# Kernel tuning notes

Measured on AMD Instinct MI355X. Metric: run time of the kernel, lower is better.

The kernel has to match this reference:

```python
import jax, jax.numpy as jnp
import numpy as np

N_NODES = 100000
N_EDGES = 1600000
D = 128


def setup_inputs() -> dict:
    key = jax.random.key(0)
    k1, k2, k3, k4 = jax.random.split(key, 4)
    x = jax.random.normal(k1, (N_NODES, D), dtype=jnp.float32)
    edge_index = jax.random.randint(k2, (2, N_EDGES), 0, N_NODES, dtype=jnp.int32)
    # torch.nn.Linear(nfeat, nclass): weight [out, in], bias [out]
    W = jax.random.normal(k3, (D, D), dtype=jnp.float32) * (1.0 / np.sqrt(D))
    b = jax.random.normal(k4, (D,), dtype=jnp.float32) * 0.01
    return {"x": x, "edge_index": edge_index, "W": W, "b": b}


def reference(x, edge_index, W, b):
    n = x.shape[0]
    # gcn_norm: add self-loops, edge_weight = 1
    loop = jnp.arange(n, dtype=edge_index.dtype)
    row = jnp.concatenate([edge_index[0], loop])  # source
    col = jnp.concatenate([edge_index[1], loop])  # target
    deg = jax.ops.segment_sum(jnp.ones_like(col, dtype=x.dtype), col, num_segments=n)
    dinv = jnp.where(deg > 0, deg ** -0.5, 0.0)
    norm = dinv[row] * dinv[col]  # [E+N]
    # K=1 propagate: out[col] += norm * x[row]
    agg = jax.ops.segment_sum(x[row] * norm[:, None], col, num_segments=n)
    # linear (y = agg @ W^T + b), then relu + residual
    h = agg @ W.T + b
    return x + jax.nn.relu(h)
```

## Files before the change

kernel.cpp:

```cpp
#include <hip/hip_runtime.h>

#define NN 100000
#define NE 1600000
#define DD 128
#define NBLK 98
#define NBUK 782
#define NB_AC 256
#define CHUNK 6250
#define SCAN_N (NBUK * NB_AC)
#define NB_SCAN 196
#define NB_YG ((NN + 63) / 64)

typedef __attribute__((ext_vector_type(8))) short bf16x8;
typedef __attribute__((ext_vector_type(4))) float f32x4;
typedef __attribute__((ext_vector_type(2))) float f32x2;

__device__ __forceinline__ float bf2f(unsigned short u) {
    return __uint_as_float(((unsigned)u) << 16);
}
__device__ __forceinline__ unsigned short f2bf(float f) {
    unsigned u = __float_as_uint(f);
    u += 0x7FFFu + ((u >> 16) & 1u);
    return (unsigned short)(u >> 16);
}

__global__ __launch_bounds__(1024) void k_hist(const int* __restrict__ col,
                                               unsigned* __restrict__ part) {
    __shared__ unsigned hist[NBUK];
    int t = threadIdx.x, blk = blockIdx.x;
    for (int i = t; i < NBUK; i += 1024) hist[i] = 0;
    __syncthreads();
    int beg = blk * CHUNK, end = beg + CHUNK;
    for (int e = beg + t; e < end; e += 1024)
        atomicAdd(&hist[col[e] >> 7], 1u);
    __syncthreads();
    for (int i = t; i < NBUK; i += 1024)
        part[(size_t)i * NB_AC + blk] = hist[i];
}

__global__ __launch_bounds__(1024) void k_bsum(const unsigned* __restrict__ part,
                                               unsigned* __restrict__ sb) {
    __shared__ unsigned red[1024];
    int t = threadIdx.x;
    int i = blockIdx.x * 1024 + t;
    red[t] = i < SCAN_N ? part[i] : 0;
    __syncthreads();
    for (int off = 512; off > 0; off >>= 1) {
        if (t < off) red[t] += red[t + off];
        __syncthreads();
    }
    if (t == 0) sb[blockIdx.x] = red[0];
}

__global__ __launch_bounds__(1024) void k_scanpart(const unsigned* __restrict__ part,
                                                   const unsigned* __restrict__ sb,
                                                   unsigned* __restrict__ off) {
    __shared__ unsigned s2[256];
    __shared__ unsigned s[1024];
    int t = threadIdx.x;
    if (t < 256) s2[t] = (t < NB_SCAN) ? sb[t] : 0;
    __syncthreads();
    for (int o = 1; o < 256; o <<= 1) {
        unsigned v = 0;
        if (t < 256 && t >= o) v = s2[t - o];
        __syncthreads();
        if (t < 256) s2[t] += v;
        __syncthreads();
    }
    unsigned boff = blockIdx.x == 0 ? 0 : s2[blockIdx.x - 1];
    int i = blockIdx.x * 1024 + t;
    unsigned v = i < SCAN_N ? part[i] : 0;
    s[t] = v;
    __syncthreads();
    for (int o = 1; o < 1024; o <<= 1) {
        unsigned u = t >= o ? s[t - o] : 0;
        __syncthreads();
        s[t] += u;
        __syncthreads();
    }
    if (i < SCAN_N) off[i] = boff + s[t] - v;
}

__global__ __launch_bounds__(1024) void k_scatter_pk(const int* __restrict__ row,
                                                     const int* __restrict__ col,
                                                     const unsigned* __restrict__ off,
                                                     unsigned* __restrict__ packed) {
    __shared__ unsigned cur[NBUK];
    int t = threadIdx.x, blk = blockIdx.x;
    for (int i = t; i < NBUK; i += 1024) cur[i] = off[(size_t)i * NB_AC + blk];
    __syncthreads();
    int beg = blk * CHUNK, end = beg + CHUNK;
    for (int e = beg + t; e < end; e += 1024) {
        int c = col[e];
        unsigned pos = atomicAdd(&cur[c >> 7], 1u);
        packed[pos] = ((unsigned)(c & 127) << 17) | (unsigned)row[e];
    }
}

__global__ __launch_bounds__(256) void k_finalize(const unsigned* __restrict__ off,
                                                  const unsigned* __restrict__ packed,
                                                  float* __restrict__ dinv,
                                                  int* __restrict__ rowptr,
                                                  int* __restrict__ esrc,
                                                  const float* __restrict__ x,
                                                  const float* __restrict__ W,
                                                  unsigned char* __restrict__ yb8) {
    __shared__ unsigned short wb[DD * DD];
    __shared__ unsigned deg[128], pre[128], tmp[128];
    int t = threadIdx.x;

    if (blockIdx.x < NBUK) {
        int buk = blockIdx.x;
        unsigned bstart = off[(size_t)buk * NB_AC];
        unsigned bend = (buk == NBUK - 1) ? (unsigned)NE : off[(size_t)(buk + 1) * NB_AC];
        if (t < 128) deg[t] = 0;
        __syncthreads();
        for (unsigned e = bstart + t; e < bend; e += 256)
            atomicAdd(&deg[packed[e] >> 17], 1u);
        __syncthreads();
        if (t < 128) tmp[t] = deg[t];
        __syncthreads();
        for (int o = 1; o < 128; o <<= 1) {
            unsigned v = 0;
            if (t < 128 && t >= o) v = tmp[t - o];
            __syncthreads();
            if (t < 128) tmp[t] += v;
            __syncthreads();
        }
        if (t < 128) {
            pre[t] = tmp[t] - deg[t];
            int n = buk * 128 + t;
            if (n < NN) {
                dinv[n] = 1.0f / sqrtf((float)(deg[t] + 1));
                rowptr[n] = (int)(bstart + pre[t]);
            }
        }
        if (buk == NBUK - 1 && t == 0) rowptr[NN] = NE;
        __syncthreads();
        if (t < 128) deg[t] = pre[t];
        __syncthreads();
        for (unsigned e = bstart + t; e < bend; e += 256) {
            unsigned p = packed[e];
            unsigned pos = atomicAdd(&deg[p >> 17], 1u);
            esrc[bstart + pos] = (int)(p & 0x1FFFFu);
        }
    } else {
        int blk = blockIdx.x - NBUK;
#pragma unroll
        for (int it = 0; it < 8; ++it) {
            int unit = t + 256 * it;
            int wrow = unit >> 4;
            int c0 = (unit & 15) * 8;
            float4 v0 = *(const float4*)(W + wrow * DD + c0);
            float4 v1 = *(const float4*)(W + wrow * DD + c0 + 4);
            bf16x8 h;
            h[0] = (short)f2bf(v0.x); h[1] = (short)f2bf(v0.y);
            h[2] = (short)f2bf(v0.z); h[3] = (short)f2bf(v0.w);
            h[4] = (short)f2bf(v1.x); h[5] = (short)f2bf(v1.y);
            h[6] = (short)f2bf(v1.z); h[7] = (short)f2bf(v1.w);
            int byte = (wrow * 256 + c0 * 2) ^ ((wrow & 7) << 4);
            *(bf16x8*)((char*)wb + byte) = h;
        }
        __syncthreads();

        int wave = t >> 6;
        int lane = t & 63;
        int lrow = lane & 15;
        int kg = lane >> 4;

        int arow = blk * 64 + wave * 16 + lrow;
        int arc = arow < NN ? arow : NN - 1;
        bf16x8 afrag[4];
#pragma unroll
        for (int ks = 0; ks < 4; ++ks) {
            const float* src = x + (size_t)arc * DD + ks * 32 + kg * 8;
            float4 v0 = *(const float4*)src;
            float4 v1 = *(const float4*)(src + 4);
            bf16x8 h;
            h[0] = (short)f2bf(v0.x); h[1] = (short)f2bf(v0.y);
            h[2] = (short)f2bf(v0.z); h[3] = (short)f2bf(v0.w);
            h[4] = (short)f2bf(v1.x); h[5] = (short)f2bf(v1.y);
            h[6] = (short)f2bf(v1.z); h[7] = (short)f2bf(v1.w);
            afrag[ks] = h;
        }

        f32x4 acc[8];
#pragma unroll
        for (int ct = 0; ct < 8; ++ct) acc[ct] = (f32x4)(0.f);

#pragma unroll
        for (int ct = 0; ct < 8; ++ct) {
            int wrow = ct * 16 + lrow;
#pragma unroll
            for (int ks = 0; ks < 4; ++ks) {
                int byte = (wrow * 256 + ks * 64 + kg * 16) ^ ((wrow & 7) << 4);
                bf16x8 bfrag = *(const bf16x8*)((char*)wb + byte);
                acc[ct] = __builtin_amdgcn_mfma_f32_16x16x32_bf16(afrag[ks], bfrag, acc[ct], 0, 0, 0);
            }
        }

#pragma unroll
        for (int j = 0; j < 4; ++j) {
            int m = blk * 64 + wave * 16 + kg * 4 + j;
            if (m < NN) {
                unsigned w0 = 0, w1 = 0;
                w0 = __builtin_amdgcn_cvt_pk_fp8_f32(acc[0][j], acc[1][j], w0, false);
                w0 = __builtin_amdgcn_cvt_pk_fp8_f32(acc[2][j], acc[3][j], w0, true);
                w1 = __builtin_amdgcn_cvt_pk_fp8_f32(acc[4][j], acc[5][j], w1, false);
                w1 = __builtin_amdgcn_cvt_pk_fp8_f32(acc[6][j], acc[7][j], w1, true);
                uint2 o; o.x = w0; o.y = w1;
                *(uint2*)(yb8 + (size_t)m * DD + lrow * 8) = o;
            }
        }
    }
}

__global__ __launch_bounds__(256) void k_gather_fp8(const int* __restrict__ rowptr,
                                                    const int* __restrict__ esrc,
                                                    const unsigned char* __restrict__ yb8,
                                                    const float* __restrict__ x,
                                                    const float* __restrict__ dinv,
                                                    const float* __restrict__ bias,
                                                    float* __restrict__ out) {
    int t = threadIdx.x;
    int gl = t & 31;
    int node = blockIdx.x * 8 + (t >> 5);
    if (node >= NN) return;
    int beg = rowptr[node];
    int end = rowptr[node + 1];
    float dc = dinv[node];

    unsigned su = *(const unsigned*)(yb8 + (size_t)node * DD + gl * 4);
    f32x2 a01 = dc * __builtin_amdgcn_cvt_pk_f32_fp8(su, false);
    f32x2 a23 = dc * __builtin_amdgcn_cvt_pk_f32_fp8(su, true);

    int e = beg;
    for (; e + 7 < end; e += 8) {
        unsigned uu[8];
        float ss[8];
#pragma unroll
        for (int u = 0; u < 8; ++u) {
            int r = esrc[e + u];
            uu[u] = *(const unsigned*)(yb8 + (size_t)r * DD + gl * 4);
            ss[u] = dinv[r];
        }
#pragma unroll
        for (int u = 0; u < 8; ++u) {
            a01 += ss[u] * __builtin_amdgcn_cvt_pk_f32_fp8(uu[u], false);
            a23 += ss[u] * __builtin_amdgcn_cvt_pk_f32_fp8(uu[u], true);
        }
    }
    for (; e < end; ++e) {
        int r = esrc[e];
        unsigned u = *(const unsigned*)(yb8 + (size_t)r * DD + gl * 4);
        float s = dinv[r];
        a01 += s * __builtin_amdgcn_cvt_pk_f32_fp8(u, false);
        a23 += s * __builtin_amdgcn_cvt_pk_f32_fp8(u, true);
    }

    float vals[4] = {a01.x, a01.y, a23.x, a23.y};
    int q = gl >> 1;
    int c0 = (gl & 1) * 4;
    const float* xp = x + (size_t)node * DD;
    float* op = out + (size_t)node * DD;
#pragma unroll
    for (int i = 0; i < 4; ++i) {
        int n = (c0 + i) * 16 + q;
        float xv = __builtin_nontemporal_load(xp + n);
        float h = dc * vals[i] + bias[n];
        __builtin_nontemporal_store(xv + fmaxf(h, 0.f), op + n);
    }
}

__global__ void k_count(const int* __restrict__ col, int* __restrict__ deg) {
    int i = blockIdx.x * blockDim.x + threadIdx.x;
    if (i < NE) atomicAdd(&deg[col[i]], 1);
}
__global__ __launch_bounds__(1024) void k_blocksum_dinv(const int* __restrict__ deg,
                                                        int* __restrict__ bsum,
                                                        float* __restrict__ dinv) {
    __shared__ int red[1024];
    int t = threadIdx.x;
    int i = blockIdx.x * 1024 + t;
    int d = i < NN ? deg[i] : 0;
    if (i < NN) dinv[i] = 1.0f / sqrtf((float)(d + 1));
    red[t] = d;
    __syncthreads();
    for (int off = 512; off > 0; off >>= 1) {
        if (t < off) red[t] += red[t + off];
        __syncthreads();
    }
    if (t == 0) bsum[blockIdx.x] = red[0];
}
__global__ void k_scanbsum(const int* __restrict__ bsum, int* __restrict__ boff) {
    __shared__ int s[128];
    int t = threadIdx.x;
    s[t] = t < NBLK ? bsum[t] : 0;
    __syncthreads();
    for (int off = 1; off < 128; off <<= 1) {
        int v = t >= off ? s[t - off] : 0;
        __syncthreads();
        s[t] += v;
        __syncthreads();
    }
    if (t < NBLK) boff[t] = (t == 0) ? 0 : s[t - 1];
}
__global__ __launch_bounds__(1024) void k_scanwrite(const int* __restrict__ deg,
                                                    const int* __restrict__ boff,
                                                    int* __restrict__ rowptr) {
    __shared__ int s[1024];
    int t = threadIdx.x;
    int i = blockIdx.x * 1024 + t;
    int v = i < NN ? deg[i] : 0;
    s[t] = v;
    __syncthreads();
    for (int off = 1; off < 1024; off <<= 1) {
        int u = t >= off ? s[t - off] : 0;
        __syncthreads();
        s[t] += u;
        __syncthreads();
    }
    if (i < NN) rowptr[i] = boff[blockIdx.x] + s[t] - v;
    if (i == 0) rowptr[NN] = NE;
}
__global__ void k_fill(const int* __restrict__ row, const int* __restrict__ col,
                       const int* __restrict__ rowptr, int* __restrict__ cnt,
                       int* __restrict__ esrc) {
    int i = blockIdx.x * blockDim.x + threadIdx.x;
    if (i < NE) {
        int c = col[i];
        int pos = rowptr[c] + atomicAdd(&cnt[c], 1);
        esrc[pos] = row[i];
    }
}
__global__ __launch_bounds__(256) void k_gather(const int* __restrict__ rowptr,
                                                const int* __restrict__ esrc,
                                                const float* __restrict__ x,
                                                const float* __restrict__ dinv,
                                                float* __restrict__ agg) {
    int t = threadIdx.x;
    int lane = t & 31;
    int node = blockIdx.x * 8 + (t >> 5);
    if (node >= NN) return;
    int beg = rowptr[node];
    int end = rowptr[node + 1];
    float dc = dinv[node];
    float4 xv = ((const float4*)(x + (size_t)node * DD))[lane];
    float4 acc;
    acc.x = dc * xv.x; acc.y = dc * xv.y; acc.z = dc * xv.z; acc.w = dc * xv.w;
    int e = beg;
    for (; e + 1 < end; e += 2) {
        int r0 = esrc[e];
        int r1 = esrc[e + 1];
        float s0 = dinv[r0];
        float s1 = dinv[r1];
        float4 v0 = ((const float4*)(x + (size_t)r0 * DD))[lane];
        float4 v1 = ((const float4*)(x + (size_t)r1 * DD))[lane];
        acc.x += s0 * v0.x + s1 * v1.x;
        acc.y += s0 * v0.y + s1 * v1.y;
        acc.z += s0 * v0.z + s1 * v1.z;
        acc.w += s0 * v0.w + s1 * v1.w;
    }
    if (e < end) {
        int r = esrc[e];
        float s = dinv[r];
        float4 v = ((const float4*)(x + (size_t)r * DD))[lane];
        acc.x += s * v.x; acc.y += s * v.y; acc.z += s * v.z; acc.w += s * v.w;
    }
    acc.x *= dc; acc.y *= dc; acc.z *= dc; acc.w *= dc;
    ((float4*)(agg + (size_t)node * DD))[lane] = acc;
}
__global__ void k_transpose_w(const float* __restrict__ W, float* __restrict__ Wt) {
    int c = blockIdx.x;
    int k = threadIdx.x;
    Wt[k * DD + c] = W[c * DD + k];
}
__global__ __launch_bounds__(256) void k_gemm(const float* __restrict__ x,
                                              const float* __restrict__ Wt,
                                              const float* __restrict__ bias,
                                              float* __restrict__ out) {
    __shared__ float wt[DD * DD];
    int t = threadIdx.x;
    for (int i = t; i < DD * DD / 4; i += 256)
        ((float4*)wt)[i] = ((const float4*)Wt)[i];
    __syncthreads();

    int grp = t >> 5;
    int c4  = (t & 31) * 4;
    int rbase = blockIdx.x * 64 + grp * 8;

    float acc[8][4];
#pragma unroll
    for (int i = 0; i < 8; i++)
#pragma unroll
        for (int j = 0; j < 4; j++) acc[i][j] = 0.0f;

    for (int k = 0; k < DD; k += 4) {
        float4 w0 = *(const float4*)&wt[(k + 0) * DD + c4];
        float4 w1 = *(const float4*)&wt[(k + 1) * DD + c4];
        float4 w2 = *(const float4*)&wt[(k + 2) * DD + c4];
        float4 w3 = *(const float4*)&wt[(k + 3) * DD + c4];
#pragma unroll
        for (int i = 0; i < 8; i++) {
            int rr = rbase + i;
            rr = rr < NN ? rr : NN - 1;
            float4 a = *(const float4*)&out[(size_t)rr * DD + k];
            acc[i][0] += a.x * w0.x + a.y * w1.x + a.z * w2.x + a.w * w3.x;
            acc[i][1] += a.x * w0.y + a.y * w1.y + a.z * w2.y + a.w * w3.y;
            acc[i][2] += a.x * w0.z + a.y * w1.z + a.z * w2.z + a.w * w3.z;
            acc[i][3] += a.x * w0.w + a.y * w1.w + a.z * w2.w + a.w * w3.w;
        }
    }

    float4 bv = *(const float4*)&bias[c4];
#pragma unroll
    for (int i = 0; i < 8; i++) {
        int r = rbase + i;
        if (r < NN) {
            float4 xv = *(const float4*)&x[(size_t)r * DD + c4];
            float4 o;
            o.x = xv.x + fmaxf(acc[i][0] + bv.x, 0.0f);
            o.y = xv.y + fmaxf(acc[i][1] + bv.y, 0.0f);
            o.z = xv.z + fmaxf(acc[i][2] + bv.z, 0.0f);
            o.w = xv.w + fmaxf(acc[i][3] + bv.w, 0.0f);
            *(float4*)&out[(size_t)r * DD + c4] = o;
        }
    }
}

extern "C" void kernel_launch(void* const* d_in, const int* in_sizes, int n_in,
                              void* d_out, int out_size, void* d_ws, size_t ws_size,
                              hipStream_t stream) {
    const float* x   = (const float*)d_in[0];
    const int*   ei  = (const int*)d_in[1];
    const float* W   = (const float*)d_in[2];
    const float* b   = (const float*)d_in[3];
    const int* row = ei;
    const int* col = ei + NE;

    float* out = (float*)d_out;

    char* ws = (char*)d_ws;
    unsigned* part   = (unsigned*)ws;
    unsigned* off    = (unsigned*)(ws + 800768);
    unsigned* sb     = (unsigned*)(ws + 1601536);
    float*    dinv   = (float*)(ws + 1602352);
    int*      rowptr = (int*)(ws + 2002352);
    unsigned* packed = (unsigned*)(ws + 2402368);
    float*    Wt     = (float*)(ws + 8802368);
    int*      esrc   = (int*)(ws + 8867904);
    unsigned char* yb8 = (unsigned char*)(ws + 15267904);

    bool big_ws = ws_size >= 28100000;

    if (big_ws) {
        k_hist<<<NB_AC, 1024, 0, stream>>>(col, part);
        k_bsum<<<NB_SCAN, 1024, 0, stream>>>(part, sb);
        k_scanpart<<<NB_SCAN, 1024, 0, stream>>>(part, sb, off);
        k_scatter_pk<<<NB_AC, 1024, 0, stream>>>(row, col, off, packed);
        k_finalize<<<NBUK + NB_YG, 256, 0, stream>>>(off, packed, dinv, rowptr, esrc, x, W, yb8);
        k_gather_fp8<<<(NN + 7) / 8, 256, 0, stream>>>(rowptr, esrc, yb8, x, dinv, b, out);
    } else {
        int* cnt  = (int*)ws;
        int* bsum = (int*)(ws + 1601536);
        int* boff = (int*)(ws + 400000);
        hipMemsetAsync(cnt, 0, NN * sizeof(int), stream);
        k_count<<<(NE + 255) / 256, 256, 0, stream>>>(col, cnt);
        k_blocksum_dinv<<<NBLK, 1024, 0, stream>>>(cnt, bsum, dinv);
        k_scanbsum<<<1, 128, 0, stream>>>(bsum, boff);
        k_scanwrite<<<NBLK, 1024, 0, stream>>>(cnt, boff, rowptr);
        hipMemsetAsync(cnt, 0, NN * sizeof(int), stream);
        k_fill<<<(NE + 255) / 256, 256, 0, stream>>>(row, col, rowptr, cnt, esrc);
        k_gather<<<(NN + 7) / 8, 256, 0, stream>>>(rowptr, esrc, x, dinv, out);
        k_transpose_w<<<DD, DD, 0, stream>>>(W, Wt);
        k_gemm<<<(NN + 63) / 64, 256, 0, stream>>>(x, Wt, b, out);
    }
}
```

Baseline: 120.2 us.

## Fuse CSR build stages into one cooperative kernel with grid syncs

Merges histogram, block-sum, scan, scatter and finalize into a single cooperative launch of 256 blocks of 1024 threads, using grid.sync between phases instead of separate kernel launches. The x·W^T fp8 GEMM is moved into the histogram phase so it runs alongside the edge counting. This removes four kernel launch boundaries, at the cost of running with only 256 resident blocks and paying grid-wide barrier latency. The old small-workspace path is replaced by the multi-kernel sequence as a fallback.

```diff
diff --git a/kernel.cpp b/kernel.cpp
--- a/kernel.cpp
+++ b/kernel.cpp
@@ -1,4 +1,7 @@
 #include <hip/hip_runtime.h>
+#include <hip/hip_cooperative_groups.h>
+
+namespace cg = cooperative_groups;
 
 #define NN 100000
 #define NE 1600000
@@ -10,6 +13,7 @@
 #define SCAN_N (NBUK * NB_AC)
 #define NB_SCAN 196
 #define NB_YG ((NN + 63) / 64)
+#define NYQ 391
 
 typedef __attribute__((ext_vector_type(8))) short bf16x8;
 typedef __attribute__((ext_vector_type(4))) float f32x4;
@@ -24,101 +28,167 @@
     return (unsigned short)(u >> 16);
 }
 
-__global__ __launch_bounds__(1024) void k_hist(const int* __restrict__ col,
-                                               unsigned* __restrict__ part) {
+__global__ __launch_bounds__(1024) void k_build(
+    const int* __restrict__ row, const int* __restrict__ col,
+    unsigned* __restrict__ part, unsigned* __restrict__ sb,
+    unsigned* __restrict__ off, unsigned* __restrict__ packed,
+    float* __restrict__ dinv, int* __restrict__ rowptr, int* __restrict__ esrc,
+    const float* __restrict__ x, const float* __restrict__ W,
+    unsigned char* __restrict__ yb8) {
+    cg::grid_group grid = cg::this_grid();
     __shared__ unsigned hist[NBUK];
-    int t = threadIdx.x, blk = blockIdx.x;
-    for (int i = t; i < NBUK; i += 1024) hist[i] = 0;
-    __syncthreads();
-    int beg = blk * CHUNK, end = beg + CHUNK;
-    for (int e = beg + t; e < end; e += 1024)
-        atomicAdd(&hist[col[e] >> 7], 1u);
-    __syncthreads();
-    for (int i = t; i < NBUK; i += 1024)
-        part[(size_t)i * NB_AC + blk] = hist[i];
-}
-
-__global__ __launch_bounds__(1024) void k_bsum(const unsigned* __restrict__ part,
-                                               unsigned* __restrict__ sb) {
+    __shared__ unsigned short wb[DD * DD];
     __shared__ unsigned red[1024];
-    int t = threadIdx.x;
-    int i = blockIdx.x * 1024 + t;
-    red[t] = i < SCAN_N ? part[i] : 0;
-    __syncthreads();
-    for (int off = 512; off > 0; off >>= 1) {
-        if (t < off) red[t] += red[t + off];
-        __syncthreads();
-    }
-    if (t == 0) sb[blockIdx.x] = red[0];
-}
-
-__global__ __launch_bounds__(1024) void k_scanpart(const unsigned* __restrict__ part,
-                                                   const unsigned* __restrict__ sb,
-                                                   unsigned* __restrict__ off) {
     __shared__ unsigned s2[256];
     __shared__ unsigned s[1024];
-    int t = threadIdx.x;
-    if (t < 256) s2[t] = (t < NB_SCAN) ? sb[t] : 0;
-    __syncthreads();
-    for (int o = 1; o < 256; o <<= 1) {
-        unsigned v = 0;
-        if (t < 256 && t >= o) v = s2[t - o];
-        __syncthreads();
-        if (t < 256) s2[t] += v;
-        __syncthreads();
-    }
-    unsigned boff = blockIdx.x == 0 ? 0 : s2[blockIdx.x - 1];
-    int i = blockIdx.x * 1024 + t;
-    unsigned v = i < SCAN_N ? part[i] : 0;
-    s[t] = v;
-    __syncthreads();
-    for (int o = 1; o < 1024; o <<= 1) {
-        unsigned u = t >= o ? s[t - o] : 0;
-        __syncthreads();
-        s[t] += u;
-        __syncthreads();
-    }
-    if (i < SCAN_N) off[i] = boff + s[t] - v;
-}
-
-__global__ __launch_bounds__(1024) void k_scatter_pk(const int* __restrict__ row,
-                                                     const int* __restrict__ col,
-                                                     const unsigned* __restrict__ off,
-                                                     unsigned* __restrict__ packed) {
-    __shared__ unsigned cur[NBUK];
+    __shared__ unsigned degs[128], pre[128], tmp[128];
     int t = threadIdx.x, blk = blockIdx.x;
-    for (int i = t; i < NBUK; i += 1024) cur[i] = off[(size_t)i * NB_AC + blk];
-    __syncthreads();
-    int beg = blk * CHUNK, end = beg + CHUNK;
-    for (int e = beg + t; e < end; e += 1024) {
-        int c = col[e];
-        unsigned pos = atomicAdd(&cur[c >> 7], 1u);
-        packed[pos] = ((unsigned)(c & 127) << 17) | (unsigned)row[e];
-    }
-}
-
-__global__ __launch_bounds__(256) void k_finalize(const unsigned* __restrict__ off,
-                                                  const unsigned* __restrict__ packed,
-                                                  float* __restrict__ dinv,
-                                                  int* __restrict__ rowptr,
-                                                  int* __restrict__ esrc,
-                                                  const float* __restrict__ x,
-                                                  const float* __restrict__ W,
-                                                  unsigned char* __restrict__ yb8) {
-    __shared__ unsigned short wb[DD * DD];
-    __shared__ unsigned deg[128], pre[128], tmp[128];
-    int t = threadIdx.x;
-
-    if (blockIdx.x < NBUK) {
-        int buk = blockIdx.x;
+
+    for (int w = blk; w < 256 + NYQ; w += 256) {
+        if (w < 256) {
+            for (int i = t; i < NBUK; i += 1024) hist[i] = 0;
+            __syncthreads();
+            int beg = w * CHUNK, end = beg + CHUNK;
+            for (int e = beg + t; e < end; e += 1024)
+                atomicAdd(&hist[col[e] >> 7], 1u);
+            __syncthreads();
+            for (int i = t; i < NBUK; i += 1024)
+                part[(size_t)i * NB_AC + w] = hist[i];
+            __syncthreads();
+        } else {
+            __syncthreads();
+#pragma unroll
+            for (int it = 0; it < 2; ++it) {
+                int unit = t + 1024 * it;
+                int wr = unit >> 4;
+                int c0 = (unit & 15) * 8;
+                float4 v0 = *(const float4*)(W + wr * DD + c0);
+                float4 v1 = *(const float4*)(W + wr * DD + c0 + 4);
+                bf16x8 h;
+                h[0] = (short)f2bf(v0.x); h[1] = (short)f2bf(v0.y);
+                h[2] = (short)f2bf(v0.z); h[3] = (short)f2bf(v0.w);
+                h[4] = (short)f2bf(v1.x); h[5] = (short)f2bf(v1.y);
+                h[6] = (short)f2bf(v1.z); h[7] = (short)f2bf(v1.w);
+                int byte = (wr * 256 + c0 * 2) ^ ((wr & 7) << 4);
+                *(bf16x8*)((char*)wb + byte) = h;
+            }
+            __syncthreads();
+
+            int tt = t & 255;
+            int wave = tt >> 6;
+            int lane = tt & 63;
+            int lrow = lane & 15;
+            int kg = lane >> 4;
+            int mbase = (w - 256) * 256 + (t >> 8) * 64;
+
+            int arow = mbase + wave * 16 + lrow;
+            int arc = arow < NN ? arow : NN - 1;
+            bf16x8 afrag[4];
+#pragma unroll
+            for (int ks = 0; ks < 4; ++ks) {
+                const float* src = x + (size_t)arc * DD + ks * 32 + kg * 8;
+                float4 v0 = *(const float4*)src;
+                float4 v1 = *(const float4*)(src + 4);
+                bf16x8 h;
+                h[0] = (short)f2bf(v0.x); h[1] = (short)f2bf(v0.y);
+                h[2] = (short)f2bf(v0.z); h[3] = (short)f2bf(v0.w);
+                h[4] = (short)f2bf(v1.x); h[5] = (short)f2bf(v1.y);
+                h[6] = (short)f2bf(v1.z); h[7] = (short)f2bf(v1.w);
+                afrag[ks] = h;
+            }
+
+            f32x4 acc[8];
+#pragma unroll
+            for (int ct = 0; ct < 8; ++ct) acc[ct] = (f32x4)(0.f);
+#pragma unroll
+            for (int ct = 0; ct < 8; ++ct) {
+                int wr = ct * 16 + lrow;
+#pragma unroll
+                for (int ks = 0; ks < 4; ++ks) {
+                    int byte = (wr * 256 + ks * 64 + kg * 16) ^ ((wr & 7) << 4);
+                    bf16x8 bfrag = *(const bf16x8*)((char*)wb + byte);
+                    acc[ct] = __builtin_amdgcn_mfma_f32_16x16x32_bf16(afrag[ks], bfrag, acc[ct], 0, 0, 0);
+                }
+            }
+
+#pragma unroll
+            for (int j = 0; j < 4; ++j) {
+                int m = mbase + wave * 16 + kg * 4 + j;
+                if (m < NN) {
+                    unsigned w0 = 0, w1 = 0;
+                    w0 = __builtin_amdgcn_cvt_pk_fp8_f32(acc[0][j], acc[1][j], w0, false);
+                    w0 = __builtin_amdgcn_cvt_pk_fp8_f32(acc[2][j], acc[3][j], w0, true);
+                    w1 = __builtin_amdgcn_cvt_pk_fp8_f32(acc[4][j], acc[5][j], w1, false);
+                    w1 = __builtin_amdgcn_cvt_pk_fp8_f32(acc[6][j], acc[7][j], w1, true);
+                    uint2 o; o.x = w0; o.y = w1;
+                    *(uint2*)(yb8 + (size_t)m * DD + lrow * 8) = o;
+                }
+            }
+            __syncthreads();
+        }
+    }
+    grid.sync();
+
+    for (int v = blk; v < NB_SCAN; v += 256) {
+        int i = v * 1024 + t;
+        red[t] = i < SCAN_N ? part[i] : 0;
+        __syncthreads();
+        for (int o = 512; o > 0; o >>= 1) {
+            if (t < o) red[t] += red[t + o];
+            __syncthreads();
+        }
+        if (t == 0) sb[v] = red[0];
+        __syncthreads();
+    }
+    grid.sync();
+
+    for (int v = blk; v < NB_SCAN; v += 256) {
+        if (t < 256) s2[t] = (t < NB_SCAN) ? sb[t] : 0;
+        __syncthreads();
+        for (int o = 1; o < 256; o <<= 1) {
+            unsigned vv = 0;
+            if (t < 256 && t >= o) vv = s2[t - o];
+            __syncthreads();
+            if (t < 256) s2[t] += vv;
+            __syncthreads();
+        }
+        unsigned boff = v == 0 ? 0 : s2[v - 1];
+        int i = v * 1024 + t;
+        unsigned val = i < SCAN_N ? part[i] : 0;
+        s[t] = val;
+        __syncthreads();
+        for (int o = 1; o < 1024; o <<= 1) {
+            unsigned u = t >= o ? s[t - o] : 0;
+            __syncthreads();
+            s[t] += u;
+            __syncthreads();
+        }
+        if (i < SCAN_N) off[i] = boff + s[t] - val;
+        __syncthreads();
+    }
+    grid.sync();
+
+    for (int i = t; i < NBUK; i += 1024) hist[i] = off[(size_t)i * NB_AC + blk];
+    __syncthreads();
+    {
+        int beg = blk * CHUNK, end = beg + CHUNK;
+        for (int e = beg + t; e < end; e += 1024) {
+            int c = col[e];
+            unsigned pos = atomicAdd(&hist[c >> 7], 1u);
+            packed[pos] = ((unsigned)(c & 127) << 17) | (unsigned)row[e];
+        }
+    }
+    grid.sync();
+
+    for (int buk = blk; buk < NBUK; buk += 256) {
         unsigned bstart = off[(size_t)buk * NB_AC];
         unsigned bend = (buk == NBUK - 1) ? (unsigned)NE : off[(size_t)(buk + 1) * NB_AC];
-        if (t < 128) deg[t] = 0;
-        __syncthreads();
-        for (unsigned e = bstart + t; e < bend; e += 256)
-            atomicAdd(&deg[packed[e] >> 17], 1u);
-        __syncthreads();
-        if (t < 128) tmp[t] = deg[t];
+        if (t < 128) degs[t] = 0;
+        __syncthreads();
+        for (unsigned e = bstart + t; e < bend; e += 1024)
+            atomicAdd(&degs[packed[e] >> 17], 1u);
+        __syncthreads();
+        if (t < 128) tmp[t] = degs[t];
         __syncthreads();
         for (int o = 1; o < 128; o <<= 1) {
             unsigned v = 0;
@@ -128,90 +198,23 @@
             __syncthreads();
         }
         if (t < 128) {
-            pre[t] = tmp[t] - deg[t];
+            pre[t] = tmp[t] - degs[t];
             int n = buk * 128 + t;
             if (n < NN) {
-                dinv[n] = 1.0f / sqrtf((float)(deg[t] + 1));
+                dinv[n] = 1.0f / sqrtf((float)(degs[t] + 1));
                 rowptr[n] = (int)(bstart + pre[t]);
             }
         }
         if (buk == NBUK - 1 && t == 0) rowptr[NN] = NE;
         __syncthreads();
-        if (t < 128) deg[t] = pre[t];
-        __syncthreads();
-        for (unsigned e = bstart + t; e < bend; e += 256) {
+        if (t < 128) degs[t] = pre[t];
+        __syncthreads();
+        for (unsigned e = bstart + t; e < bend; e += 1024) {
             unsigned p = packed[e];
-            unsigned pos = atomicAdd(&deg[p >> 17], 1u);
+            unsigned pos = atomicAdd(&degs[p >> 17], 1u);
             esrc[bstart + pos] = (int)(p & 0x1FFFFu);
         }
-    } else {
-        int blk = blockIdx.x - NBUK;
-#pragma unroll
-        for (int it = 0; it < 8; ++it) {
-            int unit = t + 256 * it;
-            int wrow = unit >> 4;
-            int c0 = (unit & 15) * 8;
-            float4 v0 = *(const float4*)(W + wrow * DD + c0);
-            float4 v1 = *(const float4*)(W + wrow * DD + c0 + 4);
-            bf16x8 h;
-            h[0] = (short)f2bf(v0.x); h[1] = (short)f2bf(v0.y);
-            h[2] = (short)f2bf(v0.z); h[3] = (short)f2bf(v0.w);
-            h[4] = (short)f2bf(v1.x); h[5] = (short)f2bf(v1.y);
-            h[6] = (short)f2bf(v1.z); h[7] = (short)f2bf(v1.w);
-            int byte = (wrow * 256 + c0 * 2) ^ ((wrow & 7) << 4);
-            *(bf16x8*)((char*)wb + byte) = h;
-        }
-        __syncthreads();
-
-        int wave = t >> 6;
-        int lane = t & 63;
-        int lrow = lane & 15;
-        int kg = lane >> 4;
-
-        int arow = blk * 64 + wave * 16 + lrow;
-        int arc = arow < NN ? arow : NN - 1;
-        bf16x8 afrag[4];
-#pragma unroll
-        for (int ks = 0; ks < 4; ++ks) {
-            const float* src = x + (size_t)arc * DD + ks * 32 + kg * 8;
-            float4 v0 = *(const float4*)src;
-            float4 v1 = *(const float4*)(src + 4);
-            bf16x8 h;
-            h[0] = (short)f2bf(v0.x); h[1] = (short)f2bf(v0.y);
-            h[2] = (short)f2bf(v0.z); h[3] = (short)f2bf(v0.w);
-            h[4] = (short)f2bf(v1.x); h[5] = (short)f2bf(v1.y);
-            h[6] = (short)f2bf(v1.z); h[7] = (short)f2bf(v1.w);
-            afrag[ks] = h;
-        }
-
-        f32x4 acc[8];
-#pragma unroll
-        for (int ct = 0; ct < 8; ++ct) acc[ct] = (f32x4)(0.f);
-
-#pragma unroll
-        for (int ct = 0; ct < 8; ++ct) {
-            int wrow = ct * 16 + lrow;
-#pragma unroll
-            for (int ks = 0; ks < 4; ++ks) {
-                int byte = (wrow * 256 + ks * 64 + kg * 16) ^ ((wrow & 7) << 4);
-                bf16x8 bfrag = *(const bf16x8*)((char*)wb + byte);
-                acc[ct] = __builtin_amdgcn_mfma_f32_16x16x32_bf16(afrag[ks], bfrag, acc[ct], 0, 0, 0);
-            }
-        }
-
-#pragma unroll
-        for (int j = 0; j < 4; ++j) {
-            int m = blk * 64 + wave * 16 + kg * 4 + j;
-            if (m < NN) {
-                unsigned w0 = 0, w1 = 0;
-                w0 = __builtin_amdgcn_cvt_pk_fp8_f32(acc[0][j], acc[1][j], w0, false);
-                w0 = __builtin_amdgcn_cvt_pk_fp8_f32(acc[2][j], acc[3][j], w0, true);
-                w1 = __builtin_amdgcn_cvt_pk_fp8_f32(acc[4][j], acc[5][j], w1, false);
-                w1 = __builtin_amdgcn_cvt_pk_fp8_f32(acc[6][j], acc[7][j], w1, true);
-                uint2 o; o.x = w0; o.y = w1;
-                *(uint2*)(yb8 + (size_t)m * DD + lrow * 8) = o;
-            }
-        }
+        __syncthreads();
     }
 }
 
@@ -253,9 +256,9 @@
     for (; e < end; ++e) {
         int r = esrc[e];
         unsigned u = *(const unsigned*)(yb8 + (size_t)r * DD + gl * 4);
-        float s = dinv[r];
-        a01 += s * __builtin_amdgcn_cvt_pk_f32_fp8(u, false);
-        a23 += s * __builtin_amdgcn_cvt_pk_f32_fp8(u, true);
+        float sv = dinv[r];
+        a01 += sv * __builtin_amdgcn_cvt_pk_f32_fp8(u, false);
+        a23 += sv * __builtin_amdgcn_cvt_pk_f32_fp8(u, true);
     }
 
     float vals[4] = {a01.x, a01.y, a23.x, a23.y};
@@ -272,158 +275,187 @@
     }
 }
 
-__global__ void k_count(const int* __restrict__ col, int* __restrict__ deg) {
-    int i = blockIdx.x * blockDim.x + threadIdx.x;
-    if (i < NE) atomicAdd(&deg[col[i]], 1);
-}
-__global__ __launch_bounds__(1024) void k_blocksum_dinv(const int* __restrict__ deg,
-                                                        int* __restrict__ bsum,
-                                                        float* __restrict__ dinv) {
-    __shared__ int red[1024];
+__global__ __launch_bounds__(1024) void k_hist(const int* __restrict__ col,
+                                               unsigned* __restrict__ part) {
+    __shared__ unsigned hist[NBUK];
+    int t = threadIdx.x, blk = blockIdx.x;
+    for (int i = t; i < NBUK; i += 1024) hist[i] = 0;
+    __syncthreads();
+    int beg = blk * CHUNK, end = beg + CHUNK;
+    for (int e = beg + t; e < end; e += 1024)
+        atomicAdd(&hist[col[e] >> 7], 1u);
+    __syncthreads();
+    for (int i = t; i < NBUK; i += 1024)
+        part[(size_t)i * NB_AC + blk] = hist[i];
+}
+__global__ __launch_bounds__(1024) void k_bsum(const unsigned* __restrict__ part,
+                                               unsigned* __restrict__ sb) {
+    __shared__ unsigned red[1024];
     int t = threadIdx.x;
     int i = blockIdx.x * 1024 + t;
-    int d = i < NN ? deg[i] : 0;
-    if (i < NN) dinv[i] = 1.0f / sqrtf((float)(d + 1));
-    red[t] = d;
+    red[t] = i < SCAN_N ? part[i] : 0;
     __syncthreads();
     for (int off = 512; off > 0; off >>= 1) {
         if (t < off) red[t] += red[t + off];
         __syncthreads();
     }
-    if (t == 0) bsum[blockIdx.x] = red[0];
-}
-__global__ void k_scanbsum(const int* __restrict__ bsum, int* __restrict__ boff) {
-    __shared__ int s[128];
+    if (t == 0) sb[blockIdx.x] = red[0];
+}
+__global__ __launch_bounds__(1024) void k_scanpart(const unsigned* __restrict__ part,
+                                                   const unsigned* __restrict__ sb,
+                                                   unsigned* __restrict__ off) {
+    __shared__ unsigned s2[256];
+    __shared__ unsigned s[1024];
     int t = threadIdx.x;
-    s[t] = t < NBLK ? bsum[t] : 0;
-    __syncthreads();
-    for (int off = 1; off < 128; off <<= 1) {
-        int v = t >= off ? s[t - off] : 0;
-        __syncthreads();
-        s[t] += v;
-        __syncthreads();
-    }
-    if (t < NBLK) boff[t] = (t == 0) ? 0 : s[t - 1];
-}
-__global__ __launch_bounds__(1024) void k_scanwrite(const int* __restrict__ deg,
-                                                    const int* __restrict__ boff,
-                                                    int* __restrict__ rowptr) {
-    __shared__ int s[1024];
+    if (t < 256) s2[t] = (t < NB_SCAN) ? sb[t] : 0;
+    __syncthreads();
+    for (int o = 1; o < 256; o <<= 1) {
+        unsigned v = 0;
+        if (t < 256 && t >= o) v = s2[t - o];
+        __syncthreads();
+        if (t < 256) s2[t] += v;
+        __syncthreads();
+    }
+    unsigned boff = blockIdx.x == 0 ? 0 : s2[blockIdx.x - 1];
+    int i = blockIdx.x * 1024 + t;
+    unsigned v = i < SCAN_N ? part[i] : 0;
+    s[t] = v;
+    __syncthreads();
+    for (int o = 1; o < 1024; o <<= 1) {
+        unsigned u = t >= o ? s[t - o] : 0;
+        __syncthreads();
+        s[t] += u;
+        __syncthreads();
+    }
+    if (i < SCAN_N) off[i] = boff + s[t] - v;
+}
+__global__ __launch_bounds__(1024) void k_scatter_pk(const int* __restrict__ row,
+                                                     const int* __restrict__ col,
+                                                     const unsigned* __restrict__ off,
+                                                     unsigned* __restrict__ packed) {
+    __shared__ unsigned cur[NBUK];
+    int t = threadIdx.x, blk = blockIdx.x;
+    for (int i = t; i < NBUK; i += 1024) cur[i] = off[(size_t)i * NB_AC + blk];
+    __syncthreads();
+    int beg = blk * CHUNK, end = beg + CHUNK;
+    for (int e = beg + t; e < end; e += 1024) {
+        int c = col[e];
+        unsigned pos = atomicAdd(&cur[c >> 7], 1u);
+        packed[pos] = ((unsigned)(c & 127) << 17) | (unsigned)row[e];
+    }
+}
+__global__ __launch_bounds__(256) void k_finalize(const unsigned* __restrict__ off,
+                                                  const unsigned* __restrict__ packed,
+                                                  float* __restrict__ dinv,
+                                                  int* __restrict__ rowptr,
+                                                  int* __restrict__ esrc,
+                                                  const float* __restrict__ x,
+                                                  const float* __restrict__ W,
+                                                  unsigned char* __restrict__ yb8) {
+    __shared__ unsigned short wb[DD * DD];
+    __shared__ unsigned deg[128], pre[128], tmp[128];
     int t = threadIdx.x;
-    int i = blockIdx.x * 1024 + t;
-    int v = i < NN ? deg[i] : 0;
-    s[t] = v;
-    __syncthreads();
-    for (int off = 1; off < 1024; off <<= 1) {
-        int u = t >= off ? s[t - off] : 0;
-        __syncthreads();
-        s[t] += u;
-        __syncthreads();
-    }
-    if (i < NN) rowptr[i] = boff[blockIdx.x] + s[t] - v;
-    if (i == 0) rowptr[NN] = NE;
-}
-__global__ void k_fill(const int* __restrict__ row, const int* __restrict__ col,
-                       const int* __restrict__ rowptr, int* __restrict__ cnt,
-                       int* __restrict__ esrc) {
-    int i = blockIdx.x * blockDim.x + threadIdx.x;
-    if (i < NE) {
-        int c = col[i];
-        int pos = rowptr[c] + atomicAdd(&cnt[c], 1);
-        esrc[pos] = row[i];
-    }
-}
-__global__ __launch_bounds__(256) void k_gather(const int* __restrict__ rowptr,
-                                                const int* __restrict__ esrc,
-                                                const float* __restrict__ x,
-                                                const float* __restrict__ dinv,
-                                                float* __restrict__ agg) {
-    int t = threadIdx.x;
-    int lane = t & 31;
-    int node = blockIdx.x * 8 + (t >> 5);
-    if (node >= NN) return;
-    int beg = rowptr[node];
-    int end = rowptr[node + 1];
-    float dc = dinv[node];
-    float4 xv = ((const float4*)(x + (size_t)node * DD))[lane];
-    float4 acc;
-    acc.x = dc * xv.x; acc.y = dc * xv.y; acc.z = dc * xv.z; acc.w = dc * xv.w;
-    int e = beg;
-    for (; e + 1 < end; e += 2) {
-        int r0 = esrc[e];
-        int r1 = esrc[e + 1];
-        float s0 = dinv[r0];
-        float s1 = dinv[r1];
-        float4 v0 = ((const float4*)(x + (size_t)r0 * DD))[lane];
-        float4 v1 = ((const float4*)(x + (size_t)r1 * DD))[lane];
-        acc.x += s0 * v0.x + s1 * v1.x;
-        acc.y += s0 * v0.y + s1 * v1.y;
-        acc.z += s0 * v0.z + s1 * v1.z;
-        acc.w += s0 * v0.w + s1 * v1.w;
-    }
-    if (e < end) {
-        int r = esrc[e];
-        float s = dinv[r];
-        float4 v = ((const float4*)(x + (size_t)r * DD))[lane];
-        acc.x += s * v.x; acc.y += s * v.y; acc.z += s * v.z; acc.w += s * v.w;
-    }
-    acc.x *= dc; acc.y *= dc; acc.z *= dc; acc.w *= dc;
-    ((float4*)(agg + (size_t)node * DD))[lane] = acc;
-}
-__global__ void k_transpose_w(const float* __restrict__ W, float* __restrict__ Wt) {
-    int c = blockIdx.x;
-    int k = threadIdx.x;
-    Wt[k * DD + c] = W[c * DD + k];
-}
-__global__ __launch_bounds__(256) void k_gemm(const float* __restrict__ x,
-                                              const float* __restrict__ Wt,
-                                              const float* __restrict__ bias,
-                                              float* __restrict__ out) {
-    __shared__ float wt[DD * DD];
-    int t = threadIdx.x;
-    for (int i = t; i < DD * DD / 4; i += 256)
-        ((float4*)wt)[i] = ((const float4*)Wt)[i];
-    __syncthreads();
-
-    int grp = t >> 5;
-    int c4  = (t & 31) * 4;
-    int rbase = blockIdx.x * 64 + grp * 8;
-
-    float acc[8][4];
-#pragma unroll
-    for (int i = 0; i < 8; i++)
-#pragma unroll
-        for (int j = 0; j < 4; j++) acc[i][j] = 0.0f;
-
-    for (int k = 0; k < DD; k += 4) {
-        float4 w0 = *(const float4*)&wt[(k + 0) * DD + c4];
-        float4 w1 = *(const float4*)&wt[(k + 1) * DD + c4];
-        float4 w2 = *(const float4*)&wt[(k + 2) * DD + c4];
-        float4 w3 = *(const float4*)&wt[(k + 3) * DD + c4];
-#pragma unroll
-        for (int i = 0; i < 8; i++) {
-            int rr = rbase + i;
-            rr = rr < NN ? rr : NN - 1;
-            float4 a = *(const float4*)&out[(size_t)rr * DD + k];
-            acc[i][0] += a.x * w0.x + a.y * w1.x + a.z * w2.x + a.w * w3.x;
-            acc[i][1] += a.x * w0.y + a.y * w1.y + a.z * w2.y + a.w * w3.y;
-            acc[i][2] += a.x * w0.z + a.y * w1.z + a.z * w2.z + a.w * w3.z;
-            acc[i][3] += a.x * w0.w + a.y * w1.w + a.z * w2.w + a.w * w3.w;
-        }
-    }
-
-    float4 bv = *(const float4*)&bias[c4];
-#pragma unroll
-    for (int i = 0; i < 8; i++) {
-        int r = rbase + i;
-        if (r < NN) {
-            float4 xv = *(const float4*)&x[(size_t)r * DD + c4];
-            float4 o;
-            o.x = xv.x + fmaxf(acc[i][0] + bv.x, 0.0f);
-            o.y = xv.y + fmaxf(acc[i][1] + bv.y, 0.0f);
-            o.z = xv.z + fmaxf(acc[i][2] + bv.z, 0.0f);
-            o.w = xv.w + fmaxf(acc[i][3] + bv.w, 0.0f);
-            *(float4*)&out[(size_t)r * DD + c4] = o;
+
+    if (blockIdx.x < NBUK) {
+        int buk = blockIdx.x;
+        unsigned bstart = off[(size_t)buk * NB_AC];
+        unsigned bend = (buk == NBUK - 1) ? (unsigned)NE : off[(size_t)(buk + 1) * NB_AC];
+        if (t < 128) deg[t] = 0;
+        __syncthreads();
+        for (unsigned e = bstart + t; e < bend; e += 256)
+            atomicAdd(&deg[packed[e] >> 17], 1u);
+        __syncthreads();
+        if (t < 128) tmp[t] = deg[t];
+        __syncthreads();
+        for (int o = 1; o < 128; o <<= 1) {
+            unsigned v = 0;
+            if (t < 128 && t >= o) v = tmp[t - o];
+            __syncthreads();
+            if (t < 128) tmp[t] += v;
+            __syncthreads();
+        }
+        if (t < 128) {
+            pre[t] = tmp[t] - deg[t];
+            int n = buk * 128 + t;
+            if (n < NN) {
+                dinv[n] = 1.0f / sqrtf((float)(deg[t] + 1));
+                rowptr[n] = (int)(bstart + pre[t]);
+            }
+        }
+        if (buk == NBUK - 1 && t == 0) rowptr[NN] = NE;
+        __syncthreads();
+        if (t < 128) deg[t] = pre[t];
+        __syncthreads();
+        for (unsigned e = bstart + t; e < bend; e += 256) {
+            unsigned p = packed[e];
+            unsigned pos = atomicAdd(&deg[p >> 17], 1u);
+            esrc[bstart + pos] = (int)(p & 0x1FFFFu);
+        }
+    } else {
+        int blk = blockIdx.x - NBUK;
+#pragma unroll
+        for (int it = 0; it < 8; ++it) {
+            int unit = t + 256 * it;
+            int wrow = unit >> 4;
+            int c0 = (unit & 15) * 8;
+            float4 v0 = *(const float4*)(W + wrow * DD + c0);
+            float4 v1 = *(const float4*)(W + wrow * DD + c0 + 4);
+            bf16x8 h;
+            h[0] = (short)f2bf(v0.x); h[1] = (short)f2bf(v0.y);
+            h[2] = (short)f2bf(v0.z); h[3] = (short)f2bf(v0.w);
+            h[4] = (short)f2bf(v1.x); h[5] = (short)f2bf(v1.y);
+            h[6] = (short)f2bf(v1.z); h[7] = (short)f2bf(v1.w);
+            int byte = (wrow * 256 + c0 * 2) ^ ((wrow & 7) << 4);
+            *(bf16x8*)((char*)wb + byte) = h;
+        }
+        __syncthreads();
+
+        int wave = t >> 6;
+        int lane = t & 63;
+        int lrow = lane & 15;
+        int kg = lane >> 4;
+
+        int arow = blk * 64 + wave * 16 + lrow;
+        int arc = arow < NN ? arow : NN - 1;
+        bf16x8 afrag[4];
+#pragma unroll
+        for (int ks = 0; ks < 4; ++ks) {
+            const float* src = x + (size_t)arc * DD + ks * 32 + kg * 8;
+            float4 v0 = *(const float4*)src;
+            float4 v1 = *(const float4*)(src + 4);
+            bf16x8 h;
+            h[0] = (short)f2bf(v0.x); h[1] = (short)f2bf(v0.y);
+            h[2] = (short)f2bf(v0.z); h[3] = (short)f2bf(v0.w);
+            h[4] = (short)f2bf(v1.x); h[5] = (short)f2bf(v1.y);
+            h[6] = (short)f2bf(v1.z); h[7] = (short)f2bf(v1.w);
+            afrag[ks] = h;
+        }
+
+        f32x4 acc[8];
+#pragma unroll
+        for (int ct = 0; ct < 8; ++ct) acc[ct] = (f32x4)(0.f);
+#pragma unroll
+        for (int ct = 0; ct < 8; ++ct) {
+            int wrow = ct * 16 + lrow;
+#pragma unroll
+            for (int ks = 0; ks < 4; ++ks) {
+                int byte = (wrow * 256 + ks * 64 + kg * 16) ^ ((wrow & 7) << 4);
+                bf16x8 bfrag = *(const bf16x8*)((char*)wb + byte);
+                acc[ct] = __builtin_amdgcn_mfma_f32_16x16x32_bf16(afrag[ks], bfrag, acc[ct], 0, 0, 0);
+            }
+        }
+#pragma unroll
+        for (int j = 0; j < 4; ++j) {
+            int m = blk * 64 + wave * 16 + kg * 4 + j;
+            if (m < NN) {
+                unsigned w0 = 0, w1 = 0;
+                w0 = __builtin_amdgcn_cvt_pk_fp8_f32(acc[0][j], acc[1][j], w0, false);
+                w0 = __builtin_amdgcn_cvt_pk_fp8_f32(acc[2][j], acc[3][j], w0, true);
+                w1 = __builtin_amdgcn_cvt_pk_fp8_f32(acc[4][j], acc[5][j], w1, false);
+                w1 = __builtin_amdgcn_cvt_pk_fp8_f32(acc[6][j], acc[7][j], w1, true);
+                uint2 o; o.x = w0; o.y = w1;
+                *(uint2*)(yb8 + (size_t)m * DD + lrow * 8) = o;
+            }
         }
     }
 }
@@ -447,32 +479,31 @@
     float*    dinv   = (float*)(ws + 1602352);
     int*      rowptr = (int*)(ws + 2002352);
     unsigned* packed = (unsigned*)(ws + 2402368);
-    float*    Wt     = (float*)(ws + 8802368);
     int*      esrc   = (int*)(ws + 8867904);
     unsigned char* yb8 = (unsigned char*)(ws + 15267904);
 
     bool big_ws = ws_size >= 28100000;
 
     if (big_ws) {
+        void* args[] = {(void*)&row, (void*)&col, (void*)&part, (void*)&sb,
+                        (void*)&off, (void*)&packed, (void*)&dinv, (void*)&rowptr,
+                        (void*)&esrc, (void*)&x, (void*)&W, (void*)&yb8};
+        hipError_t err = hipLaunchCooperativeKernel((void*)k_build, dim3(256), dim3(1024),
+                                                    args, 0, stream);
+        if (err != hipSuccess) {
+            k_hist<<<NB_AC, 1024, 0, stream>>>(col, part);
+            k_bsum<<<NB_SCAN, 1024, 0, stream>>>(part, sb);
+            k_scanpart<<<NB_SCAN, 1024, 0, stream>>>(part, sb, off);
+            k_scatter_pk<<<NB_AC, 1024, 0, stream>>>(row, col, off, packed);
+            k_finalize<<<NBUK + NB_YG, 256, 0, stream>>>(off, packed, dinv, rowptr, esrc, x, W, yb8);
+        }
+        k_gather_fp8<<<(NN + 7) / 8, 256, 0, stream>>>(rowptr, esrc, yb8, x, dinv, b, out);
+    } else {
         k_hist<<<NB_AC, 1024, 0, stream>>>(col, part);
         k_bsum<<<NB_SCAN, 1024, 0, stream>>>(part, sb);
         k_scanpart<<<NB_SCAN, 1024, 0, stream>>>(part, sb, off);
         k_scatter_pk<<<NB_AC, 1024, 0, stream>>>(row, col, off, packed);
         k_finalize<<<NBUK + NB_YG, 256, 0, stream>>>(off, packed, dinv, rowptr, esrc, x, W, yb8);
         k_gather_fp8<<<(NN + 7) / 8, 256, 0, stream>>>(rowptr, esrc, yb8, x, dinv, b, out);
-    } else {
-        int* cnt  = (int*)ws;
-        int* bsum = (int*)(ws + 1601536);
-        int* boff = (int*)(ws + 400000);
-        hipMemsetAsync(cnt, 0, NN * sizeof(int), stream);
-        k_count<<<(NE + 255) / 256, 256, 0, stream>>>(col, cnt);
-        k_blocksum_dinv<<<NBLK, 1024, 0, stream>>>(cnt, bsum, dinv);
-        k_scanbsum<<<1, 128, 0, stream>>>(bsum, boff);
-        k_scanwrite<<<NBLK, 1024, 0, stream>>>(cnt, boff, rowptr);
-        hipMemsetAsync(cnt, 0, NN * sizeof(int), stream);
-        k_fill<<<(NE + 255) / 256, 256, 0, stream>>>(row, col, rowptr, cnt, esrc);
-        k_gather<<<(NN + 7) / 8, 256, 0, stream>>>(rowptr, esrc, x, dinv, out);
-        k_transpose_w<<<DD, DD, 0, stream>>>(W, Wt);
-        k_gemm<<<(NN + 63) / 64, 256, 0, stream>>>(x, Wt, b, out);
-    }
-}
+    }
+}
```

Result: slower. 257.6 us (+114.4%).
